# Kernel optimization log

Hardware: AMD Instinct MI355X
Metric: run time of the kernel (lower is better)

Reference implementation:

```python
import jax, jax.numpy as jnp
import numpy as np

BN_EPS = 1e-5

def _mlp(h, w1, b1, w2, b2):
    return jax.nn.relu(h @ w1 + b1) @ w2 + b2

def _segment_mean(data, seg, num_segments):
    s = jax.ops.segment_sum(data, seg, num_segments=num_segments)
    c = jax.ops.segment_sum(jnp.ones((data.shape[0],), data.dtype), seg, num_segments=num_segments)
    return s / jnp.maximum(c, 1.0)[:, None]

def _lin_init(k, fan_in, fan_out):
    k1, k2 = jax.random.split(k)
    s = 1.0 / float(np.sqrt(fan_in))
    w = jax.random.uniform(k1, (fan_in, fan_out), jnp.float32, -s, s)
    b = jax.random.uniform(k2, (fan_out,), jnp.float32, -s, s)
    return w, b

def setup_inputs() -> dict:
    key = jax.random.key(0)
    ks = jax.random.split(key, 16)
    N, E, B = 100000, 1600000, 256
    d1, d2, d3, d5, nc = 3, 50, 15, 10, 6
    x = jax.random.normal(ks[0], (N, d1), jnp.float32)
    edge_index = jax.random.randint(ks[1], (2, E), 0, N)
    edge_attr = jax.random.normal(ks[2], (E, d1), jnp.float32)
    u = jax.random.normal(ks[3], (B, 1), jnp.float32)
    batch = jnp.sort(jax.random.randint(ks[4], (N,), 0, B))
    ew1, eb1 = _lin_init(ks[5], d1 * 3, d2)
    ew2, eb2 = _lin_init(ks[6], d2, d3)
    nw1, nb1 = _lin_init(ks[7], d1 * 6, d2)
    nw2, nb2 = _lin_init(ks[8], d2, d3)
    gw1, gb1 = _lin_init(ks[9], d3 + 1, d2)
    gw2, gb2 = _lin_init(ks[10], d2, d3)
    fc1_w, fc1_b = _lin_init(ks[11], d3, d5)
    bn_g = jnp.ones((d5,), jnp.float32)
    bn_b = jnp.zeros((d5,), jnp.float32)
    fc2_w, fc2_b = _lin_init(ks[12], d5, nc)
    return dict(x=x, edge_index=edge_index, edge_attr=edge_attr, u=u, batch=batch,
                ew1=ew1, eb1=eb1, ew2=ew2, eb2=eb2,
                nw1=nw1, nb1=nb1, nw2=nw2, nb2=nb2,
                gw1=gw1, gb1=gb1, gw2=gw2, gb2=gb2,
                fc1_w=fc1_w, fc1_b=fc1_b, bn_g=bn_g, bn_b=bn_b,
                fc2_w=fc2_w, fc2_b=fc2_b)

def reference(x, edge_index, edge_attr, u, batch,
              ew1, eb1, ew2, eb2, nw1, nb1, nw2, nb2,
              gw1, gb1, gw2, gb2, fc1_w, fc1_b, bn_g, bn_b, fc2_w, fc2_b):
    N = x.shape[0]
    B = u.shape[0]
    row, col = edge_index[0], edge_index[1]
    # edge update: cat([x[row], x[col], edge_attr]) -> MLP  => [E, d3]
    e2 = _mlp(jnp.concatenate([x[row], x[col], edge_attr], axis=1), ew1, eb1, ew2, eb2)
    # node update: cat([x[col], e2]) -> MLP -> scatter_mean over row  => [N, d3]
    h = _mlp(jnp.concatenate([x[col], e2], axis=1), nw1, nb1, nw2, nb2)
    x2 = _segment_mean(h, row, N)
    # global update: cat([u, mean_per_graph(x2)]) -> MLP  => [B, d3]
    u2 = _mlp(jnp.concatenate([u, _segment_mean(x2, batch, B)], axis=1), gw1, gb1, gw2, gb2)
    # readout: relu(cat nodes + globals), mean-pool per graph (u2 rows join their graph)
    z = jax.nn.relu(jnp.concatenate([x2, u2], axis=0))  # dropout off (eval mode)
    seg = jnp.concatenate([batch, jnp.arange(B, dtype=batch.dtype)])
    g = _segment_mean(z, seg, B)  # [B, d3]
    h1 = g @ fc1_w + fc1_b
    # BatchNorm1d in eval mode with default running stats (mean=0, var=1)
    h1 = jax.nn.relu(h1 * (bn_g / jnp.sqrt(1.0 + BN_EPS)) + bn_b)
    return jax.nn.log_softmax(h1 @ fc2_w + fc2_b, axis=1)
```

## Files before the change

kernel.cpp:

```cpp
#include <hip/hip_runtime.h>
#include <math.h>

#define D1 3
#define D2 50
#define D3 15
#define D5 10
#define NC 6
#define SCAN_B 512
#define GS 64

typedef _Float16 h2 __attribute__((ext_vector_type(2)));
typedef __fp16   fp16x2 __attribute__((ext_vector_type(2)));

__device__ __forceinline__ float fdot2(h2 a, h2 b, float c) {
#if __has_builtin(__builtin_amdgcn_fdot2)
    return __builtin_amdgcn_fdot2(a, b, c, false);
#else
    return c + (float)a[0] * (float)b[0] + (float)a[1] * (float)b[1];
#endif
}

__device__ __forceinline__ h2 pkrtz(float a, float b) {
#if __has_builtin(__builtin_amdgcn_cvt_pkrtz)
    fp16x2 r = __builtin_amdgcn_cvt_pkrtz(a, b);
    return __builtin_bit_cast(h2, r);
#else
    h2 v; v[0] = (_Float16)a; v[1] = (_Float16)b; return v;
#endif
}

__global__ __launch_bounds__(256) void deg_rank_prep_kernel(
    const int* __restrict__ ei, int* __restrict__ deg, int* __restrict__ rank, int E,
    const float* __restrict__ ew1, const float* __restrict__ nw1,
    const float* __restrict__ ew2, const float* __restrict__ nw2,
    h2* __restrict__ ew1pk, h2* __restrict__ nw1pk,
    h2* __restrict__ ew2pk, h2* __restrict__ nw2pk)
{
    int e = blockIdx.x * blockDim.x + threadIdx.x;
    if (e < E) {
        int r = ei[e];
        rank[e] = atomicAdd(&deg[r], 1);
    }
    if (blockIdx.x == 0) {
        int t = threadIdx.x;
        for (int i = t; i < D2 * 5; i += 256) {
            int j = i / 5, p = i - 5 * j;
            float a = ew1[(2 * p) * D2 + j];
            float b = (2 * p + 1 < 9) ? ew1[(2 * p + 1) * D2 + j] : 0.0f;
            h2 v; v[0] = (_Float16)a; v[1] = (_Float16)b;
            ew1pk[i] = v;
        }
        for (int i = t; i < D2 * 9; i += 256) {
            int j = i / 9, p = i - 9 * j;
            float a = nw1[(2 * p) * D2 + j];
            float b = nw1[(2 * p + 1) * D2 + j];
            h2 v; v[0] = (_Float16)a; v[1] = (_Float16)b;
            nw1pk[i] = v;
        }
        for (int i = t; i < D3 * 25; i += 256) {
            int m = i / 25, k = i - 25 * m;
            float a = ew2[(2 * k) * D3 + m];
            float b = ew2[(2 * k + 1) * D3 + m];
            h2 v; v[0] = (_Float16)a; v[1] = (_Float16)b;
            ew2pk[i] = v;
            float c = nw2[(2 * k) * D3 + m];
            float d = nw2[(2 * k + 1) * D3 + m];
            h2 w; w[0] = (_Float16)c; w[1] = (_Float16)d;
            nw2pk[i] = w;
        }
    }
}

__global__ __launch_bounds__(SCAN_B) void scan1_kernel(
    const int* __restrict__ deg, int* __restrict__ base, int* __restrict__ bsum, int N)
{
    __shared__ int sm[SCAN_B];
    int i = blockIdx.x * SCAN_B + threadIdx.x;
    int v = (i < N) ? deg[i] : 0;
    sm[threadIdx.x] = v;
    __syncthreads();
    #pragma unroll
    for (int s = 1; s < SCAN_B; s <<= 1) {
        int t = (threadIdx.x >= (unsigned)s) ? sm[threadIdx.x - s] : 0;
        __syncthreads();
        sm[threadIdx.x] += t;
        __syncthreads();
    }
    if (i < N) base[i] = sm[threadIdx.x] - v;
    if (threadIdx.x == SCAN_B - 1) bsum[blockIdx.x] = sm[threadIdx.x];
}

__global__ __launch_bounds__(SCAN_B) void scan23_kernel(
    int* __restrict__ base, const int* __restrict__ bsum, int N)
{
    int bid = blockIdx.x;
    int sum = 0;
    for (int t = (int)threadIdx.x; t < bid; t += SCAN_B) sum += bsum[t];
    #pragma unroll
    for (int s = 32; s > 0; s >>= 1) sum += __shfl_down(sum, s);
    __shared__ int ws[SCAN_B / 64];
    __shared__ int s_total;
    int lane = threadIdx.x & 63, wid = threadIdx.x >> 6;
    if (lane == 0) ws[wid] = sum;
    __syncthreads();
    if (threadIdx.x == 0) {
        int tot = 0;
        #pragma unroll
        for (int w = 0; w < SCAN_B / 64; ++w) tot += ws[w];
        s_total = tot;
    }
    __syncthreads();
    int i = bid * SCAN_B + threadIdx.x;
    if (i < N) base[i] += s_total;
}

__global__ __launch_bounds__(256, 4) void edge_mlp_fused_kernel(
    const float* __restrict__ x,
    const int*   __restrict__ ei,
    const float* __restrict__ ea,
    const h2* __restrict__ ew1pk, const float* __restrict__ eb1,
    const h2* __restrict__ ew2pk, const float* __restrict__ eb2,
    const h2* __restrict__ nw1pk, const float* __restrict__ nb1,
    const h2* __restrict__ nw2pk, const float* __restrict__ nb2,
    const int* __restrict__ base, const int* __restrict__ rank,
    unsigned int* __restrict__ hbuf16,
    int E)
{
    int e = blockIdx.x * blockDim.x + threadIdx.x;
    if (e >= E) return;

    int r = ei[e];
    int c = ei[E + e];
    int slot = base[r] + rank[e];

    float in9[9];
    in9[0] = x[3 * r + 0];
    in9[1] = x[3 * r + 1];
    in9[2] = x[3 * r + 2];
    in9[3] = x[3 * c + 0];
    in9[4] = x[3 * c + 1];
    in9[5] = x[3 * c + 2];
    in9[6] = ea[3 * e + 0];
    in9[7] = ea[3 * e + 1];
    in9[8] = ea[3 * e + 2];

    h2 inpk[5];
    inpk[0] = pkrtz(in9[0], in9[1]);
    inpk[1] = pkrtz(in9[2], in9[3]);
    inpk[2] = pkrtz(in9[4], in9[5]);
    inpk[3] = pkrtz(in9[6], in9[7]);
    inpk[4] = pkrtz(in9[8], 0.0f);

    h2 hpk[25];
    #pragma unroll
    for (int jj = 0; jj < 25; ++jj) {
        float a0 = eb1[2 * jj];
        float a1 = eb1[2 * jj + 1];
        #pragma unroll
        for (int p = 0; p < 5; ++p) {
            a0 = fdot2(inpk[p], ew1pk[(2 * jj) * 5 + p], a0);
            a1 = fdot2(inpk[p], ew1pk[(2 * jj + 1) * 5 + p], a1);
        }
        hpk[jj] = pkrtz(fmaxf(a0, 0.0f), fmaxf(a1, 0.0f));
    }

    float e2v[D3];
    #pragma unroll
    for (int m = 0; m < D3; ++m) {
        float a = eb2[m];
        #pragma unroll
        for (int k = 0; k < 25; ++k) a = fdot2(hpk[k], ew2pk[m * 25 + k], a);
        e2v[m] = a;
    }

    h2 vpk[9];
    vpk[0] = pkrtz(in9[3], in9[4]);
    vpk[1] = pkrtz(in9[5], e2v[0]);
    #pragma unroll
    for (int p = 2; p < 9; ++p) vpk[p] = pkrtz(e2v[2 * p - 3], e2v[2 * p - 2]);

    h2 h2pk[25];
    #pragma unroll
    for (int jj = 0; jj < 25; ++jj) {
        float a0 = nb1[2 * jj];
        float a1 = nb1[2 * jj + 1];
        #pragma unroll
        for (int p = 0; p < 9; ++p) {
            a0 = fdot2(vpk[p], nw1pk[(2 * jj) * 9 + p], a0);
            a1 = fdot2(vpk[p], nw1pk[(2 * jj + 1) * 9 + p], a1);
        }
        h2pk[jj] = pkrtz(fmaxf(a0, 0.0f), fmaxf(a1, 0.0f));
    }

    float acc[D3 + 1];
    #pragma unroll
    for (int m = 0; m < D3; ++m) {
        float a = nb2[m];
        #pragma unroll
        for (int k = 0; k < 25; ++k) a = fdot2(h2pk[k], nw2pk[m * 25 + k], a);
        acc[m] = a;
    }
    acc[D3] = 0.0f;

    union { h2 h[8]; uint4 u[2]; } outp;
    #pragma unroll
    for (int p = 0; p < 8; ++p) outp.h[p] = pkrtz(acc[2 * p], acc[2 * p + 1]);

    uint4* dst = (uint4*)(hbuf16 + (size_t)slot * 8);
    dst[0] = outp.u[0];
    dst[1] = outp.u[1];
}

__global__ __launch_bounds__(256) void tail_partial_kernel(
    const unsigned int* __restrict__ hbuf16,
    const int* __restrict__ deg, const int* __restrict__ base,
    const int* __restrict__ batch, int N,
    float* __restrict__ gsum)
{
    __shared__ float sacc[16 * GS];
    int tid = threadIdx.x;
    #pragma unroll
    for (int q = tid; q < 16 * GS; q += 256) sacc[q] = 0.0f;
    __syncthreads();

    int n0 = blockIdx.x * 32;
    int n  = n0 + (tid >> 3);
    int p  = tid & 7;
    int g_first = batch[n0 < N ? n0 : (N - 1)];

    if (n < N) {
        int bs = base[n];
        int d  = deg[n];
        int g  = batch[n];
        float a0 = 0.0f, a1 = 0.0f;
        const unsigned int* ptr = hbuf16 + (size_t)bs * 8 + p;
        for (int k = 0; k < d; ++k) {
            unsigned int w = ptr[(size_t)k * 8];
            h2 v = __builtin_bit_cast(h2, w);
            a0 += (float)v[0];
            a1 += (float)v[1];
        }
        float inv = 1.0f / fmaxf((float)d, 1.0f);
        float v0 = a0 * inv, v1 = a1 * inv;
        float r0 = fmaxf(v0, 0.0f), r1 = fmaxf(v1, 0.0f);
        int sl = g - g_first;
        if (sl < 16) {
            atomicAdd(&sacc[sl * GS + 2 * p],          v0);
            atomicAdd(&sacc[sl * GS + 2 * p + 1],      v1);
            atomicAdd(&sacc[sl * GS + 32 + 2 * p],     r0);
            atomicAdd(&sacc[sl * GS + 32 + 2 * p + 1], r1);
        } else {
            atomicAdd(&gsum[(size_t)g * GS + 2 * p],          v0);
            atomicAdd(&gsum[(size_t)g * GS + 2 * p + 1],      v1);
            atomicAdd(&gsum[(size_t)g * GS + 32 + 2 * p],     r0);
            atomicAdd(&gsum[(size_t)g * GS + 32 + 2 * p + 1], r1);
        }
    }
    __syncthreads();

    if (tid < GS) {
        for (int sl = 0; sl < 16; ++sl) {
            float v = sacc[sl * GS + tid];
            if (v != 0.0f) atomicAdd(&gsum[(size_t)(g_first + sl) * GS + tid], v);
        }
    }
}

__global__ __launch_bounds__(256) void final_head_kernel(
    const float* __restrict__ gsum, const int* __restrict__ batch, int N,
    const float* __restrict__ u,
    const float* __restrict__ gw1, const float* __restrict__ gb1,
    const float* __restrict__ gw2, const float* __restrict__ gb2,
    const float* __restrict__ fc1w, const float* __restrict__ fc1b,
    const float* __restrict__ bng, const float* __restrict__ bnb,
    const float* __restrict__ fc2w, const float* __restrict__ fc2b,
    float* __restrict__ out, int B)
{
    int t = blockIdx.x * blockDim.x + threadIdx.x;
    if (t >= B) return;

    int lo = 0, hi = N;
    while (lo < hi) { int m = (lo + hi) >> 1; if (batch[m] < t) lo = m + 1; else hi = m; }
    int start = lo;
    hi = N;
    while (lo < hi) { int m = (lo + hi) >> 1; if (batch[m] < t + 1) lo = m + 1; else hi = m; }
    float nct = (float)(lo - start);

    float in16[16];
    in16[0] = u[t];
    float invn = 1.0f / fmaxf(nct, 1.0f);
    #pragma unroll
    for (int j = 0; j < D3; ++j) in16[1 + j] = gsum[(size_t)t * GS + j] * invn;

    float gh[D2];
    #pragma unroll
    for (int j = 0; j < D2; ++j) {
        float a = gb1[j];
        #pragma unroll
        for (int k = 0; k < 16; ++k) a = fmaf(in16[k], gw1[k * D2 + j], a);
        gh[j] = fmaxf(a, 0.0f);
    }

    float g[D3];
    #pragma unroll
    for (int j = 0; j < D3; ++j) {
        float a = gb2[j];
        #pragma unroll
        for (int k = 0; k < D2; ++k) a = fmaf(gh[k], gw2[k * D3 + j], a);
        g[j] = (gsum[(size_t)t * GS + 32 + j] + fmaxf(a, 0.0f)) / (nct + 1.0f);
    }

    const float bnscale = 1.0f / sqrtf(1.0f + 1e-5f);
    float h1[D5];
    #pragma unroll
    for (int i = 0; i < D5; ++i) {
        float a = fc1b[i];
        #pragma unroll
        for (int k = 0; k < D3; ++k) a = fmaf(g[k], fc1w[k * D5 + i], a);
        h1[i] = fmaxf(a * (bng[i] * bnscale) + bnb[i], 0.0f);
    }

    float o[NC];
    #pragma unroll
    for (int j = 0; j < NC; ++j) {
        float a = fc2b[j];
        #pragma unroll
        for (int k = 0; k < D5; ++k) a = fmaf(h1[k], fc2w[k * NC + j], a);
        o[j] = a;
    }
    float m = o[0];
    #pragma unroll
    for (int j = 1; j < NC; ++j) m = fmaxf(m, o[j]);
    float ssum = 0.0f;
    #pragma unroll
    for (int j = 0; j < NC; ++j) ssum += expf(o[j] - m);
    float lse = m + logf(ssum);
    #pragma unroll
    for (int j = 0; j < NC; ++j) out[t * NC + j] = o[j] - lse;
}

__global__ __launch_bounds__(256) void edge_node_atomic_kernel(
    const float* __restrict__ x,
    const int*   __restrict__ ei,
    const float* __restrict__ ea,
    const float* __restrict__ ew1, const float* __restrict__ eb1,
    const float* __restrict__ ew2, const float* __restrict__ eb2,
    const float* __restrict__ nw1, const float* __restrict__ nb1,
    const float* __restrict__ nw2, const float* __restrict__ nb2,
    float* __restrict__ x2sum, float* __restrict__ cnt,
    int E)
{
    int e = blockIdx.x * blockDim.x + threadIdx.x;
    if (e >= E) return;
    int r = ei[e];
    int c = ei[E + e];
    float in9[9];
    in9[0] = x[3 * r + 0]; in9[1] = x[3 * r + 1]; in9[2] = x[3 * r + 2];
    float xc0 = x[3 * c + 0], xc1 = x[3 * c + 1], xc2 = x[3 * c + 2];
    in9[3] = xc0; in9[4] = xc1; in9[5] = xc2;
    in9[6] = ea[3 * e + 0]; in9[7] = ea[3 * e + 1]; in9[8] = ea[3 * e + 2];
    float h[D2];
    #pragma unroll
    for (int j = 0; j < D2; ++j) {
        float a = eb1[j];
        #pragma unroll
        for (int k = 0; k < 9; ++k) a = fmaf(in9[k], ew1[k * D2 + j], a);
        h[j] = fmaxf(a, 0.0f);
    }
    float e2[D3];
    #pragma unroll
    for (int j = 0; j < D3; ++j) {
        float a = eb2[j];
        #pragma unroll
        for (int k = 0; k < D2; ++k) a = fmaf(h[k], ew2[k * D3 + j], a);
        e2[j] = a;
    }
    float h2v[D2];
    #pragma unroll
    for (int j = 0; j < D2; ++j) {
        float a = nb1[j];
        a = fmaf(xc0, nw1[0 * D2 + j], a);
        a = fmaf(xc1, nw1[1 * D2 + j], a);
        a = fmaf(xc2, nw1[2 * D2 + j], a);
        #pragma unroll
        for (int k = 0; k < D3; ++k) a = fmaf(e2[k], nw1[(3 + k) * D2 + j], a);
        h2v[j] = fmaxf(a, 0.0f);
    }
    float* dst = x2sum + (size_t)r * D3;
    #pragma unroll
    for (int j = 0; j < D3; ++j) {
        float a = nb2[j];
        #pragma unroll
        for (int k = 0; k < D2; ++k) a = fmaf(h2v[k], nw2[k * D3 + j], a);
        atomicAdd(&dst[j], a);
    }
    atomicAdd(&cnt[r], 1.0f);
}

__global__ __launch_bounds__(256) void graph_sum_atomic_kernel(
    const float* __restrict__ x2sum, const float* __restrict__ cnt,
    const int* __restrict__ batch, int N,
    float* __restrict__ bx, float* __restrict__ brelu, float* __restrict__ ncnt)
{
    int b = blockIdx.x;
    int lo = 0, hi = N;
    while (lo < hi) { int m = (lo + hi) >> 1; if (batch[m] < b) lo = m + 1; else hi = m; }
    int start = lo;
    hi = N;
    while (lo < hi) { int m = (lo + hi) >> 1; if (batch[m] < b + 1) lo = m + 1; else hi = m; }
    int end = lo;
    float sx[D3], sr[D3];
    #pragma unroll
    for (int j = 0; j < D3; ++j) { sx[j] = 0.0f; sr[j] = 0.0f; }
    for (int i = start + (int)threadIdx.x; i < end; i += (int)blockDim.x) {
        float inv = 1.0f / fmaxf(cnt[i], 1.0f);
        #pragma unroll
        for (int j = 0; j < D3; ++j) {
            float v = x2sum[(size_t)i * D3 + j] * inv;
            sx[j] += v;
            sr[j] += fmaxf(v, 0.0f);
        }
    }
    #pragma unroll
    for (int j = 0; j < D3; ++j) {
        #pragma unroll
        for (int s = 32; s > 0; s >>= 1) {
            sx[j] += __shfl_down(sx[j], s);
            sr[j] += __shfl_down(sr[j], s);
        }
    }
    __shared__ float sm[4][2 * D3];
    int lane = threadIdx.x & 63, wid = threadIdx.x >> 6;
    if (lane == 0) {
        #pragma unroll
        for (int j = 0; j < D3; ++j) { sm[wid][j] = sx[j]; sm[wid][D3 + j] = sr[j]; }
    }
    __syncthreads();
    if (threadIdx.x < 2 * D3) {
        float v = sm[0][threadIdx.x] + sm[1][threadIdx.x] + sm[2][threadIdx.x] + sm[3][threadIdx.x];
        if (threadIdx.x < D3) bx[b * D3 + threadIdx.x] = v;
        else                  brelu[b * D3 + (threadIdx.x - D3)] = v;
    }
    if (threadIdx.x == 0) ncnt[b] = (float)(end - start);
}

__global__ __launch_bounds__(256) void final_kernel(
    const float* __restrict__ u,
    const float* __restrict__ gw1, const float* __restrict__ gb1,
    const float* __restrict__ gw2, const float* __restrict__ gb2,
    const float* __restrict__ fc1w, const float* __restrict__ fc1b,
    const float* __restrict__ bng, const float* __restrict__ bnb,
    const float* __restrict__ fc2w, const float* __restrict__ fc2b,
    const float* __restrict__ bx, const float* __restrict__ brelu,
    const float* __restrict__ ncnt,
    float* __restrict__ out, int B)
{
    int t = blockIdx.x * blockDim.x + threadIdx.x;
    if (t >= B) return;
    float nct = ncnt[t];
    float inv = 1.0f / fmaxf(nct, 1.0f);
    float in16[16];
    in16[0] = u[t];
    #pragma unroll
    for (int j = 0; j < D3; ++j) in16[1 + j] = bx[t * D3 + j] * inv;
    float gh[D2];
    #pragma unroll
    for (int j = 0; j < D2; ++j) {
        float a = gb1[j];
        #pragma unroll
        for (int k = 0; k < 16; ++k) a = fmaf(in16[k], gw1[k * D2 + j], a);
        gh[j] = fmaxf(a, 0.0f);
    }
    float g[D3];
    #pragma unroll
    for (int j = 0; j < D3; ++j) {
        float a = gb2[j];
        #pragma unroll
        for (int k = 0; k < D2; ++k) a = fmaf(gh[k], gw2[k * D3 + j], a);
        g[j] = (brelu[t * D3 + j] + fmaxf(a, 0.0f)) / (nct + 1.0f);
    }
    const float bnscale = 1.0f / sqrtf(1.0f + 1e-5f);
    float h1[D5];
    #pragma unroll
    for (int i = 0; i < D5; ++i) {
        float a = fc1b[i];
        #pragma unroll
        for (int k = 0; k < D3; ++k) a = fmaf(g[k], fc1w[k * D5 + i], a);
        h1[i] = fmaxf(a * (bng[i] * bnscale) + bnb[i], 0.0f);
    }
    float o[NC];
    #pragma unroll
    for (int j = 0; j < NC; ++j) {
        float a = fc2b[j];
        #pragma unroll
        for (int k = 0; k < D5; ++k) a = fmaf(h1[k], fc2w[k * NC + j], a);
        o[j] = a;
    }
    float m = o[0];
    #pragma unroll
    for (int j = 1; j < NC; ++j) m = fmaxf(m, o[j]);
    float ssum = 0.0f;
    #pragma unroll
    for (int j = 0; j < NC; ++j) ssum += expf(o[j] - m);
    float lse = m + logf(ssum);
    #pragma unroll
    for (int j = 0; j < NC; ++j) out[t * NC + j] = o[j] - lse;
}

extern "C" void kernel_launch(void* const* d_in, const int* in_sizes, int n_in,
                              void* d_out, int out_size, void* d_ws, size_t ws_size,
                              hipStream_t stream) {
    const float* x     = (const float*)d_in[0];
    const int*   ei    = (const int*)  d_in[1];
    const float* ea    = (const float*)d_in[2];
    const float* u     = (const float*)d_in[3];
    const int*   batch = (const int*)  d_in[4];
    const float* ew1 = (const float*)d_in[5];
    const float* eb1 = (const float*)d_in[6];
    const float* ew2 = (const float*)d_in[7];
    const float* eb2 = (const float*)d_in[8];
    const float* nw1 = (const float*)d_in[9];
    const float* nb1 = (const float*)d_in[10];
    const float* nw2 = (const float*)d_in[11];
    const float* nb2 = (const float*)d_in[12];
    const float* gw1 = (const float*)d_in[13];
    const float* gb1 = (const float*)d_in[14];
    const float* gw2 = (const float*)d_in[15];
    const float* gb2 = (const float*)d_in[16];
    const float* fc1w = (const float*)d_in[17];
    const float* fc1b = (const float*)d_in[18];
    const float* bng  = (const float*)d_in[19];
    const float* bnb  = (const float*)d_in[20];
    const float* fc2w = (const float*)d_in[21];
    const float* fc2b = (const float*)d_in[22];

    int N = in_sizes[0] / 3;
    int E = in_sizes[2] / 3;
    int B = in_sizes[3];
    float* out = (float*)d_out;

    int nsb = (N + SCAN_B - 1) / SCAN_B;
    const size_t WPK = 2048;

    size_t need = sizeof(h2) * WPK
                + sizeof(unsigned int) * (size_t)E * 8
                + sizeof(int) * (size_t)N
                + sizeof(float) * (size_t)B * GS
                + sizeof(int) * ((size_t)E + (size_t)N + 1024);

    if (ws_size >= need && nsb <= 1024) {
        char* p = (char*)d_ws;
        h2* ew1pk = (h2*)p;
        h2* nw1pk = ew1pk + 250;
        h2* ew2pk = nw1pk + 450;
        h2* nw2pk = ew2pk + 375;
        p += sizeof(h2) * WPK;
        unsigned int* hbuf16 = (unsigned int*)p;  p += sizeof(unsigned int) * (size_t)E * 8;
        int* deg   = (int*)p;           p += sizeof(int) * (size_t)N;
        float* gsum = (float*)p;        p += sizeof(float) * (size_t)B * GS;
        int* rank = (int*)p;            p += sizeof(int) * (size_t)E;
        int* base = (int*)p;            p += sizeof(int) * (size_t)N;
        int* bsum = (int*)p;            p += sizeof(int) * 1024;

        hipMemsetAsync(deg, 0, sizeof(int) * (size_t)N + sizeof(float) * (size_t)B * GS, stream);

        int eb = (E + 255) / 256;
        deg_rank_prep_kernel<<<eb, 256, 0, stream>>>(
            ei, deg, rank, E, ew1, nw1, ew2, nw2, ew1pk, nw1pk, ew2pk, nw2pk);

        scan1_kernel<<<nsb, SCAN_B, 0, stream>>>(deg, base, bsum, N);
        scan23_kernel<<<nsb, SCAN_B, 0, stream>>>(base, bsum, N);

        edge_mlp_fused_kernel<<<eb, 256, 0, stream>>>(
            x, ei, ea, ew1pk, eb1, ew2pk, eb2, nw1pk, nb1, nw2pk, nb2,
            base, rank, hbuf16, E);

        int ntb = (N + 31) / 32;
        tail_partial_kernel<<<ntb, 256, 0, stream>>>(
            hbuf16, deg, base, batch, N, gsum);

        int fb = (B + 255) / 256;
        final_head_kernel<<<fb, 256, 0, stream>>>(
            gsum, batch, N, u, gw1, gb1, gw2, gb2,
            fc1w, fc1b, bng, bnb, fc2w, fc2b, out, B);
    } else {
        float* x2sum = (float*)d_ws;
        float* cnt   = x2sum + (size_t)N * D3;
        float* bx    = cnt + N;
        float* brelu = bx + (size_t)B * D3;
        float* ncnt  = brelu + (size_t)B * D3;

        hipMemsetAsync(x2sum, 0, sizeof(float) * ((size_t)N * D3 + N), stream);

        int eb = (E + 255) / 256;
        edge_node_atomic_kernel<<<eb, 256, 0, stream>>>(
            x, ei, ea, ew1, eb1, ew2, eb2, nw1, nb1, nw2, nb2, x2sum, cnt, E);

        graph_sum_atomic_kernel<<<B, 256, 0, stream>>>(x2sum, cnt, batch, N, bx, brelu, ncnt);

        int fb = (B + 255) / 256;
        final_kernel<<<fb, 256, 0, stream>>>(
            u, gw1, gb1, gw2, gb2, fc1w, fc1b, bng, bnb, fc2w, fc2b,
            bx, brelu, ncnt, out, B);
    }
}
```

Baseline: 234.2 us.

## Restructure tail reduction to per-graph blocks with shuffle reductions instead of atomics

The node-mean tail kernel now launches SPLIT blocks per graph. Each block finds its graph's node range by binary search on the sorted batch array, and each thread reduces one node's incoming edge rows with 16-byte vector loads. Per-graph sums come from warp shuffles and a small shared-memory combine, so the many shared and global atomics go away and the gsum stride shrinks. The cost is fewer active threads per node, less coalesced per-thread loads, and idle lanes when a graph has fewer nodes than threads.

Result: faster. 227.1 us (-3.0%).

```diff
diff --git a/kernel.cpp b/kernel.cpp
--- a/kernel.cpp
+++ b/kernel.cpp
@@ -1,13 +1,13 @@
 #include <hip/hip_runtime.h>
 #include <math.h>
 
-#define D1 3
 #define D2 50
 #define D3 15
 #define D5 10
 #define NC 6
 #define SCAN_B 512
-#define GS 64
+#define GS 32
+#define SPLIT 4
 
 typedef _Float16 h2 __attribute__((ext_vector_type(2)));
 typedef __fp16   fp16x2 __attribute__((ext_vector_type(2)));
@@ -140,9 +140,9 @@
     in9[3] = x[3 * c + 0];
     in9[4] = x[3 * c + 1];
     in9[5] = x[3 * c + 2];
-    in9[6] = ea[3 * e + 0];
-    in9[7] = ea[3 * e + 1];
-    in9[8] = ea[3 * e + 2];
+    in9[6] = ea[3 * (size_t)e + 0];
+    in9[7] = ea[3 * (size_t)e + 1];
+    in9[8] = ea[3 * (size_t)e + 2];
 
     h2 inpk[5];
     inpk[0] = pkrtz(in9[0], in9[1]);
@@ -217,52 +217,73 @@
     const int* __restrict__ batch, int N,
     float* __restrict__ gsum)
 {
-    __shared__ float sacc[16 * GS];
+    int b = blockIdx.x / SPLIT;
+    int q = blockIdx.x % SPLIT;
     int tid = threadIdx.x;
-    #pragma unroll
-    for (int q = tid; q < 16 * GS; q += 256) sacc[q] = 0.0f;
+
+    int lo = 0, hi = N;
+    while (lo < hi) { int m = (lo + hi) >> 1; if (batch[m] < b) lo = m + 1; else hi = m; }
+    int start = lo;
+    hi = N;
+    while (lo < hi) { int m = (lo + hi) >> 1; if (batch[m] < b + 1) lo = m + 1; else hi = m; }
+    int end = lo;
+
+    int len = end - start;
+    int cs = start + (int)(((long long)len * q) / SPLIT);
+    int ce = start + (int)(((long long)len * (q + 1)) / SPLIT);
+
+    float sx[D3], sr[D3];
+    #pragma unroll
+    for (int j = 0; j < D3; ++j) { sx[j] = 0.0f; sr[j] = 0.0f; }
+
+    for (int i = cs + tid; i < ce; i += 256) {
+        int bs = base[i];
+        int d  = deg[i];
+        float acc[16];
+        #pragma unroll
+        for (int j = 0; j < 16; ++j) acc[j] = 0.0f;
+        const uint4* ptr = (const uint4*)(hbuf16 + (size_t)bs * 8);
+        for (int k = 0; k < d; ++k) {
+            uint4 w0 = ptr[2 * k];
+            uint4 w1 = ptr[2 * k + 1];
+            unsigned int ws[8] = {w0.x, w0.y, w0.z, w0.w, w1.x, w1.y, w1.z, w1.w};
+            #pragma unroll
+            for (int p = 0; p < 8; ++p) {
+                h2 v = __builtin_bit_cast(h2, ws[p]);
+                acc[2 * p]     += (float)v[0];
+                acc[2 * p + 1] += (float)v[1];
+            }
+        }
+        float inv = 1.0f / fmaxf((float)d, 1.0f);
+        #pragma unroll
+        for (int j = 0; j < D3; ++j) {
+            float v = acc[j] * inv;
+            sx[j] += v;
+            sr[j] += fmaxf(v, 0.0f);
+        }
+    }
+
+    #pragma unroll
+    for (int j = 0; j < D3; ++j) {
+        #pragma unroll
+        for (int s = 32; s > 0; s >>= 1) {
+            sx[j] += __shfl_down(sx[j], s);
+            sr[j] += __shfl_down(sr[j], s);
+        }
+    }
+
+    __shared__ float sm[4][2 * D3];
+    int lane = tid & 63, wid = tid >> 6;
+    if (lane == 0) {
+        #pragma unroll
+        for (int j = 0; j < D3; ++j) { sm[wid][j] = sx[j]; sm[wid][D3 + j] = sr[j]; }
+    }
     __syncthreads();
 
-    int n0 = blockIdx.x * 32;
-    int n  = n0 + (tid >> 3);
-    int p  = tid & 7;
-    int g_first = batch[n0 < N ? n0 : (N - 1)];
-
-    if (n < N) {
-        int bs = base[n];
-        int d  = deg[n];
-        int g  = batch[n];
-        float a0 = 0.0f, a1 = 0.0f;
-        const unsigned int* ptr = hbuf16 + (size_t)bs * 8 + p;
-        for (int k = 0; k < d; ++k) {
-            unsigned int w = ptr[(size_t)k * 8];
-            h2 v = __builtin_bit_cast(h2, w);
-            a0 += (float)v[0];
-            a1 += (float)v[1];
-        }
-        float inv = 1.0f / fmaxf((float)d, 1.0f);
-        float v0 = a0 * inv, v1 = a1 * inv;
-        float r0 = fmaxf(v0, 0.0f), r1 = fmaxf(v1, 0.0f);
-        int sl = g - g_first;
-        if (sl < 16) {
-            atomicAdd(&sacc[sl * GS + 2 * p],          v0);
-            atomicAdd(&sacc[sl * GS + 2 * p + 1],      v1);
-            atomicAdd(&sacc[sl * GS + 32 + 2 * p],     r0);
-            atomicAdd(&sacc[sl * GS + 32 + 2 * p + 1], r1);
-        } else {
-            atomicAdd(&gsum[(size_t)g * GS + 2 * p],          v0);
-            atomicAdd(&gsum[(size_t)g * GS + 2 * p + 1],      v1);
-            atomicAdd(&gsum[(size_t)g * GS + 32 + 2 * p],     r0);
-            atomicAdd(&gsum[(size_t)g * GS + 32 + 2 * p + 1], r1);
-        }
-    }
-    __syncthreads();
-
-    if (tid < GS) {
-        for (int sl = 0; sl < 16; ++sl) {
-            float v = sacc[sl * GS + tid];
-            if (v != 0.0f) atomicAdd(&gsum[(size_t)(g_first + sl) * GS + tid], v);
-        }
+    if (tid < 2 * D3) {
+        float v = sm[0][tid] + sm[1][tid] + sm[2][tid] + sm[3][tid];
+        int off = (tid < D3) ? tid : (16 + tid - D3);
+        atomicAdd(&gsum[(size_t)b * GS + off], v);
     }
 }
 
@@ -307,7 +328,7 @@
         float a = gb2[j];
         #pragma unroll
         for (int k = 0; k < D2; ++k) a = fmaf(gh[k], gw2[k * D3 + j], a);
-        g[j] = (gsum[(size_t)t * GS + 32 + j] + fmaxf(a, 0.0f)) / (nct + 1.0f);
+        g[j] = (gsum[(size_t)t * GS + 16 + j] + fmaxf(a, 0.0f)) / (nct + 1.0f);
     }
 
     const float bnscale = 1.0f / sqrtf(1.0f + 1e-5f);
@@ -556,7 +577,7 @@
         h2* nw2pk = ew2pk + 375;
         p += sizeof(h2) * WPK;
         unsigned int* hbuf16 = (unsigned int*)p;  p += sizeof(unsigned int) * (size_t)E * 8;
-        int* deg   = (int*)p;           p += sizeof(int) * (size_t)N;
+        int* deg    = (int*)p;          p += sizeof(int) * (size_t)N;
         float* gsum = (float*)p;        p += sizeof(float) * (size_t)B * GS;
         int* rank = (int*)p;            p += sizeof(int) * (size_t)E;
         int* base = (int*)p;            p += sizeof(int) * (size_t)N;
@@ -575,8 +596,7 @@
             x, ei, ea, ew1pk, eb1, ew2pk, eb2, nw1pk, nb1, nw2pk, nb2,
             base, rank, hbuf16, E);
 
-        int ntb = (N + 31) / 32;
-        tail_partial_kernel<<<ntb, 256, 0, stream>>>(
+        tail_partial_kernel<<<B * SPLIT, 256, 0, stream>>>(
             hbuf16, deg, base, batch, N, gsum);
 
         int fb = (B + 255) / 256;
```
